# Kernel tuning notes

Hardware: AMD Instinct MI355X
Metric: run time of the kernel (lower is better)

Reference implementation:

```python
import jax, jax.numpy as jnp
import numpy as np


def _apply_ring(x, angles):
    """Apply x @ R^T where R = G_0 @ G_1 @ ... @ G_{n-1} with ring planes
    (k, (k+1) % n). Equivalent to applying G_k^T to x for k = n-1 .. 0:
      x[:, k] <- c*x[:, k] - s*x[:, j]
      x[:, j] <- s*x[:, k] + c*x[:, j]
    x: [B, n], angles: [n].
    """
    n = angles.shape[0]

    def step(xT, k):
        a = angles[k]
        c, s = jnp.cos(a), jnp.sin(a)
        j = jnp.mod(k + 1, n)
        xi = xT[k]
        xj = xT[j]
        xT = xT.at[k].set(c * xi - s * xj)
        xT = xT.at[j].set(s * xi + c * xj)
        return xT, None

    ks = jnp.arange(n - 1, -1, -1)  # reverse order: R^T = G_{n-1}^T ... G_0^T
    xT, _ = jax.lax.scan(step, x.T, ks)  # carry is [n, B]
    return xT.T


def setup_inputs() -> dict:
    key = jax.random.key(0)
    k_x, k_e, k_d = jax.random.split(key, 3)
    B, n, num_blocks = 8192, 1024, 4
    return {
        "x": jax.random.normal(k_x, (B, n), dtype=jnp.float32),
        "angles_enc": jax.random.normal(k_e, (num_blocks, n), dtype=jnp.float32),
        "angles_dec": jax.random.normal(k_d, (num_blocks, n), dtype=jnp.float32),
        "hidden_weight": jnp.zeros((1,), dtype=jnp.float32),
        "hidden_state": jnp.zeros((n,), dtype=jnp.float32),
    }


def reference(x, angles_enc, angles_dec, hidden_weight, hidden_state):
    num_blocks = angles_enc.shape[0]
    b = x
    for blk in range(num_blocks):
        b = _apply_ring(b, angles_enc[blk])
    # recurrent blend; weight uses the detached hidden_weight (original uses
    # numpy on .detach()), so stop_gradient matches the original semantics.
    w = jax.nn.sigmoid(jax.lax.stop_gradient(hidden_weight[0]))
    bottleneck = (1.0 - w) * b + w * hidden_state[None, :]
    out = bottleneck
    for blk in range(num_blocks):
        out = _apply_ring(out, angles_dec[blk])
    return (bottleneck, out)
```

## Files before the change

### kernel.cpp

```cpp
#include <hip/hip_runtime.h>
#include <math.h>

#define N_COLS 1024
#define NRINGS 8

#define TPR    32
#define CHUNK  32
#define PAIRS_PER_BLOCK 8

#define F_OFF   16384
#define A_OFF   24576
#define AUX_OFF 24832
#define WS_FLOATS 24848

typedef const __attribute__((address_space(1))) float4* gas_f4;
typedef __attribute__((address_space(3))) void* las_ptr;

__global__ __launch_bounds__(256)
void ced_setup(const float* __restrict__ ae,
               const float* __restrict__ ad,
               float* __restrict__ ws)
{
    __shared__ float2 ls[256];
    const int r   = blockIdx.x >> 2;
    const int b   = blockIdx.x & 3;
    const int tid = threadIdx.x;
    const int k   = (b << 8) + tid;
    const float* ang = (r < 4) ? (ae + (r << 10)) : (ad + ((r - 4) << 10));

    float sv, cv;
    sincosf(ang[k], &sv, &cv);
    if (k == N_COLS - 1) {
        ((float2*)(ws + AUX_OFF))[r] = make_float2(cv, sv);
        cv = 0.f; sv = -1.f;
    }
    ls[tid] = make_float2(cv, sv);
    __syncthreads();

    if (!(tid & 1)) {
        float2 e0 = ls[tid], e1 = ls[tid + 1];
        int t  = k >> 5;
        int jp = (k & 31) >> 1;
        ((float4*)ws)[(r*16 + jp)*32 + t] = make_float4(e0.x, e0.y, e1.x, e1.y);
    }

    if (tid < 64) {
        const int lt = tid >> 3;
        const int q  = tid & 7;
        const int t  = (b << 3) + lt;
        const int j0 = lt * CHUNK + 4 * q;
        float2 e0 = ls[j0], e1 = ls[j0+1], e2 = ls[j0+2], e3 = ls[j0+3];

        float f3 = e3.x;       float P = -e3.y;
        float f2 = e2.x * P;   P *= -e2.y;
        float f1 = e1.x * P;   P *= -e1.y;
        float f0 = e0.x * P;   P *= -e0.y;

        float ip = P;
        #pragma unroll
        for (int d = 1; d < 8; d <<= 1) {
            float tmp = __shfl_down(ip, d);
            if (q + d < 8) ip *= tmp;
        }
        float ex = __shfl_down(ip, 1);
        if (q == 7) ex = 1.f;
        f0 *= ex; f1 *= ex; f2 *= ex; f3 *= ex;

        ((float4*)(ws + F_OFF))[(r*8 + q)*32 + t] = make_float4(f0, f1, f2, f3);
        if (q == 0) ws[A_OFF + r*TPR + t] = ip;
    }
}

__global__ __launch_bounds__(256, 2)
void ced_main(const float* __restrict__ x,
              const float* __restrict__ ws,
              const float* __restrict__ hw,
              const float* __restrict__ hs,
              float* __restrict__ out, int B)
{
    __shared__ float4 sCS[2][1024];
    __shared__ float4 sF [2][512];
    __shared__ float4 sA4[64];
    __shared__ float4 sAux4[4];

    const float4* CSg = (const float4*)ws;
    const float4* Fg  = (const float4*)(ws + F_OFF);

    const int tid  = threadIdx.x;
    const int lane = tid & 63;
    const int t    = lane & 31;
    const int groupBase = lane & 32;
    const int pairRow = blockIdx.x * PAIRS_PER_BLOCK + (tid >> 5);
    const size_t rowA = (size_t)(2 * pairRow) * N_COLS;
    const size_t rowB = rowA + N_COLS;

    #pragma unroll
    for (int m = 0; m < 4; ++m)
        __builtin_amdgcn_global_load_lds((gas_f4)(CSg + m*256 + tid),
                                         (las_ptr)&sCS[0][m*256 + tid], 16, 0, 0);
    #pragma unroll
    for (int m = 0; m < 2; ++m)
        __builtin_amdgcn_global_load_lds((gas_f4)(Fg + m*256 + tid),
                                         (las_ptr)&sF[0][m*256 + tid], 16, 0, 0);

    if (tid < 64)              sA4[tid]        = ((const float4*)(ws + A_OFF))[tid];
    if (tid >= 64 && tid < 68) sAux4[tid - 64] = ((const float4*)(ws + AUX_OFF))[tid - 64];

    float ya[CHUNK], yb[CHUNK];
    {
        const float4* xa = (const float4*)(x + rowA + t * CHUNK);
        const float4* xb = (const float4*)(x + rowB + t * CHUNK);
        #pragma unroll
        for (int i = 0; i < 8; ++i) {
            float4 va = xa[i], vb = xb[i];
            ya[4*i] = va.x; ya[4*i+1] = va.y; ya[4*i+2] = va.z; ya[4*i+3] = va.w;
            yb[4*i] = vb.x; yb[4*i+1] = vb.y; yb[4*i+2] = vb.z; yb[4*i+3] = vb.w;
        }
    }

    const float w   = 1.f / (1.f + expf(-hw[0]));
    const float omw = 1.f - w;

    __syncthreads();

    const float*  As   = (const float*)sA4;
    const float2* Auxs = (const float2*)sAux4;

    #pragma unroll 1
    for (int p = 0; p < 4; ++p) {
        if (p < 3) {
            const int nb = (p + 1) & 1;
            const float4* gc = CSg + (p + 1) * 1024;
            const float4* gf = Fg  + (p + 1) * 512;
            #pragma unroll
            for (int m = 0; m < 4; ++m)
                __builtin_amdgcn_global_load_lds((gas_f4)(gc + m*256 + tid),
                                                 (las_ptr)&sCS[nb][m*256 + tid], 16, 0, 0);
            #pragma unroll
            for (int m = 0; m < 2; ++m)
                __builtin_amdgcn_global_load_lds((gas_f4)(gf + m*256 + tid),
                                                 (las_ptr)&sF[nb][m*256 + tid], 16, 0, 0);
        }

        const int buf = p & 1;
        #pragma unroll
        for (int lr = 0; lr < 2; ++lr) {
            const int rr = 2 * p + lr;

            if (p == 2 && lr == 0) {
                float4* oa = (float4*)(out + rowA + t * CHUNK);
                float4* ob = (float4*)(out + rowB + t * CHUNK);
                const float4* hp = (const float4*)(hs + t * CHUNK);
                #pragma unroll
                for (int i = 0; i < 8; ++i) {
                    float4 h = hp[i];
                    float4 na, nb2;
                    na.x  = fmaf(omw, ya[4*i+0], w * h.x);
                    na.y  = fmaf(omw, ya[4*i+1], w * h.y);
                    na.z  = fmaf(omw, ya[4*i+2], w * h.z);
                    na.w  = fmaf(omw, ya[4*i+3], w * h.w);
                    nb2.x = fmaf(omw, yb[4*i+0], w * h.x);
                    nb2.y = fmaf(omw, yb[4*i+1], w * h.y);
                    nb2.z = fmaf(omw, yb[4*i+2], w * h.z);
                    nb2.w = fmaf(omw, yb[4*i+3], w * h.w);
                    oa[i] = na; ob[i] = nb2;
                    ya[4*i+0] = na.x;  ya[4*i+1] = na.y;  ya[4*i+2] = na.z;  ya[4*i+3] = na.w;
                    yb[4*i+0] = nb2.x; yb[4*i+1] = nb2.y; yb[4*i+2] = nb2.z; yb[4*i+3] = nb2.w;
                }
            }

            const float4* csL = &sCS[buf][lr * 512];
            const float4* fL  = &sF [buf][lr * 256];
            const float2  cN  = Auxs[rr];
            const float   saI = As[rr * TPR + t];

            float y0a = __shfl(ya[0],       groupBase);
            float yNa = __shfl(ya[CHUNK-1], groupBase + 31);
            float y0b = __shfl(yb[0],       groupBase);
            float yNb = __shfl(yb[CHUNK-1], groupBase + 31);
            float CinitA = cN.x * yNa - cN.y * y0a;
            float CinitB = cN.x * yNb - cN.y * y0b;
            float x0nA   = fmaf(cN.y, yNa, cN.x * y0a);
            float x0nB   = fmaf(cN.y, yNb, cN.x * y0b);
            if (t == 0) { ya[0] = x0nA; yb[0] = x0nB; }

            float carA = 0.f, carB = 0.f, ztA = 0.f, ztB = 0.f;
            #pragma unroll
            for (int jp = CHUNK/2 - 1; jp >= 0; --jp) {
                float4 cs4 = csL[jp * 32 + t];
                const int j1 = 2*jp + 1;
                float z1a = fmaf(cs4.w, ya[j1], cs4.z * carA);
                float z1b = fmaf(cs4.w, yb[j1], cs4.z * carB);
                carA = fmaf(-cs4.w, carA, cs4.z * ya[j1]);
                carB = fmaf(-cs4.w, carB, cs4.z * yb[j1]);
                if (j1 == CHUNK - 1) { ztA = z1a; ztB = z1b; }
                else                 { ya[j1+1] = z1a; yb[j1+1] = z1b; }
                const int j0 = 2*jp;
                float z0a = fmaf(cs4.y, ya[j0], cs4.x * carA);
                float z0b = fmaf(cs4.y, yb[j0], cs4.x * carB);
                carA = fmaf(-cs4.y, carA, cs4.x * ya[j0]);
                carB = fmaf(-cs4.y, carB, cs4.x * yb[j0]);
                ya[j0+1] = z0a; yb[j0+1] = z0b;
            }

            float sa = saI;
            float sbA = carA, sbB = carB;
            #pragma unroll
            for (int d = 1; d < TPR; d <<= 1) {
                float a2  = __shfl_down(sa,  d);
                float b2a = __shfl_down(sbA, d);
                float b2b = __shfl_down(sbB, d);
                if (t + d < TPR) {
                    sbA = fmaf(sa, b2a, sbA);
                    sbB = fmaf(sa, b2b, sbB);
                    sa *= a2;
                }
            }
            float ea  = __shfl_down(sa,  1);
            float ebA = __shfl_down(sbA, 1);
            float ebB = __shfl_down(sbB, 1);
            float zfA = fmaf(sa, CinitA, sbA);
            float zfB = fmaf(sa, CinitB, sbB);
            float CinA = (t == TPR - 1) ? CinitA : fmaf(ea, CinitA, ebA);
            float CinB = (t == TPR - 1) ? CinitB : fmaf(ea, CinitB, ebB);

            #pragma unroll
            for (int qi = CHUNK/4 - 1; qi >= 0; --qi) {
                float4 f4 = fL[qi * 32 + t];
                const int j = 4*qi;
                if (j + 3 == CHUNK - 1) { ztA = fmaf(f4.w, CinA, ztA);
                                          ztB = fmaf(f4.w, CinB, ztB); }
                else                    { ya[j+4] = fmaf(f4.w, CinA, ya[j+4]);
                                          yb[j+4] = fmaf(f4.w, CinB, yb[j+4]); }
                ya[j+3] = fmaf(f4.z, CinA, ya[j+3]);  yb[j+3] = fmaf(f4.z, CinB, yb[j+3]);
                ya[j+2] = fmaf(f4.y, CinA, ya[j+2]);  yb[j+2] = fmaf(f4.y, CinB, yb[j+2]);
                ya[j+1] = fmaf(f4.x, CinA, ya[j+1]);  yb[j+1] = fmaf(f4.x, CinB, yb[j+1]);
            }

            float upA = __shfl_up(ztA, 1);
            float upB = __shfl_up(ztB, 1);
            ya[0] = (t == 0) ? zfA : upA;
            yb[0] = (t == 0) ? zfB : upB;
        }

        if (p < 3) __syncthreads();
    }

    float4* oa = (float4*)(out + (size_t)B * N_COLS + rowA + t * CHUNK);
    float4* ob = (float4*)(out + (size_t)B * N_COLS + rowB + t * CHUNK);
    #pragma unroll
    for (int i = 0; i < 8; ++i) {
        oa[i] = make_float4(ya[4*i], ya[4*i+1], ya[4*i+2], ya[4*i+3]);
        ob[i] = make_float4(yb[4*i], yb[4*i+1], yb[4*i+2], yb[4*i+3]);
    }
}

__global__ __launch_bounds__(256, 2)
void ced_fallback(const float* __restrict__ x,
                  const float* __restrict__ ae,
                  const float* __restrict__ ad,
                  const float* __restrict__ hw,
                  const float* __restrict__ hs,
                  float* __restrict__ out, int B)
{
    __shared__ float2 s_cs[NRINGS * 64 * 16];
    __shared__ float  s_A [NRINGS * 16];
    __shared__ float2 s_aux[NRINGS];

    const int tid = threadIdx.x;
    for (int i = 0; i < 32; ++i) {
        int idx = i * 256 + tid;
        int r   = idx >> 10;
        int k   = idx & 1023;
        const float* ang = (r < 4) ? (ae + (r << 10)) : (ad + ((r - 4) << 10));
        float sv, cv;
        sincosf(ang[k], &sv, &cv);
        int t = k >> 6, j = k & 63;
        float2 e = make_float2(cv, sv);
        if (k == 1023) { s_aux[r] = e; e = make_float2(0.f, -1.f); }
        s_cs[(r * 64 + j) * 16 + t] = e;
    }
    __syncthreads();
    if (tid < NRINGS * 16) {
        int r = tid >> 4, t = tid & 15;
        float p = 1.f;
        for (int j = 0; j < 64; ++j) p *= -s_cs[(r * 64 + j) * 16 + t].y;
        s_A[tid] = p;
    }
    __syncthreads();

    const int lane      = tid & 63;
    const int g         = lane >> 4;
    const int t         = lane & 15;
    const int groupBase = lane & 48;
    const int row       = blockIdx.x * 16 + (tid >> 6) * 4 + g;

    const float* xr = x + (size_t)row * N_COLS + t * 64;
    float y[64];
    #pragma unroll
    for (int i = 0; i < 16; ++i) {
        float4 v = ((const float4*)xr)[i];
        y[4*i] = v.x; y[4*i+1] = v.y; y[4*i+2] = v.z; y[4*i+3] = v.w;
    }
    const float w   = 1.f / (1.f + expf(-hw[0]));
    const float omw = 1.f - w;

    for (int r = 0; r < NRINGS; ++r) {
        if (r == 4) {
            float4* ob = (float4*)(out + (size_t)row * N_COLS + t * 64);
            const float4* hp = (const float4*)(hs + t * 64);
            #pragma unroll
            for (int i = 0; i < 16; ++i) {
                float4 h = hp[i];
                float4 bn;
                bn.x = fmaf(omw, y[4*i+0], w * h.x);
                bn.y = fmaf(omw, y[4*i+1], w * h.y);
                bn.z = fmaf(omw, y[4*i+2], w * h.z);
                bn.w = fmaf(omw, y[4*i+3], w * h.w);
                ob[i] = bn;
                y[4*i+0] = bn.x; y[4*i+1] = bn.y; y[4*i+2] = bn.z; y[4*i+3] = bn.w;
            }
        }
        const float2* csr = s_cs + r * 64 * 16;
        const float2  cN  = s_aux[r];
        float y0 = __shfl(y[0],  groupBase);
        float yN = __shfl(y[63], groupBase + 15);
        float Cinit = cN.x * yN - cN.y * y0;
        float x0n   = fmaf(cN.y, yN, cN.x * y0);
        if (t == 0) y[0] = x0n;

        float carry = 0.f, ztmp = 0.f;
        #pragma unroll
        for (int j = 63; j >= 0; --j) {
            float2 cs = csr[j * 16 + t];
            float z   = fmaf(cs.y, y[j], cs.x * carry);
            carry     = fmaf(-cs.y, carry, cs.x * y[j]);
            if (j == 63) ztmp = z; else y[j + 1] = z;
        }
        float sa = s_A[r * 16 + t], sb = carry;
        #pragma unroll
        for (int d = 1; d < 16; d <<= 1) {
            float a2 = __shfl_down(sa, d);
            float b2 = __shfl_down(sb, d);
            if (t + d < 16) { sb = fmaf(sa, b2, sb); sa *= a2; }
        }
        float ea = __shfl_down(sa, 1);
        float eb = __shfl_down(sb, 1);
        float z0  = fmaf(sa, Cinit, sb);
        float Cin = (t == 15) ? Cinit : fmaf(ea, Cinit, eb);

        float P = 1.f;
        #pragma unroll
        for (int j = 63; j >= 0; --j) {
            float2 cs = csr[j * 16 + t];
            float f = cs.x * P;
            P = -cs.y * P;
            if (j == 63) ztmp = fmaf(f, Cin, ztmp);
            else         y[j + 1] = fmaf(f, Cin, y[j + 1]);
        }
        float up = __shfl_up(ztmp, 1);
        y[0] = (t == 0) ? z0 : up;
    }

    float4* oo = (float4*)(out + (size_t)B * N_COLS + (size_t)row * N_COLS + t * 64);
    #pragma unroll
    for (int i = 0; i < 16; ++i)
        oo[i] = make_float4(y[4*i], y[4*i+1], y[4*i+2], y[4*i+3]);
}

extern "C" void kernel_launch(void* const* d_in, const int* in_sizes, int n_in,
                              void* d_out, int out_size, void* d_ws, size_t ws_size,
                              hipStream_t stream) {
    const float* x  = (const float*)d_in[0];
    const float* ae = (const float*)d_in[1];
    const float* ad = (const float*)d_in[2];
    const float* hw = (const float*)d_in[3];
    const float* hs = (const float*)d_in[4];
    float* out = (float*)d_out;
    const int B = in_sizes[0] / N_COLS;

    if (ws_size >= WS_FLOATS * sizeof(float)) {
        hipLaunchKernelGGL(ced_setup, dim3(32), dim3(256), 0, stream,
                           ae, ad, (float*)d_ws);
        hipLaunchKernelGGL(ced_main, dim3(B / (2 * PAIRS_PER_BLOCK)), dim3(256), 0, stream,
                           x, (const float*)d_ws, hw, hs, out, B);
    } else {
        hipLaunchKernelGGL(ced_fallback, dim3(B / 16), dim3(256), 0, stream,
                           x, ae, ad, hw, hs, out, B);
    }
}
```

Before: 125.4 us.

## Remap ring scan to one row per wavefront with 64 lanes of 16 columns

Switches the main kernel from two rows per 32-lane half-wave (32 columns per lane) to one row per full 64-lane wavefront with 16 columns per lane. Blocks grow to 512 threads with per-ring double-buffered coefficient staging (a barrier per ring instead of per pair of rings). The setup kernel's coefficient layout and prefix products are rewritten for the new chunking. This cuts registers per thread and raises occupancy and parallelism, but the cross-lane scan gains a sixth shuffle step and runs on all 64 lanes, and the rings no longer share two rows per lane.

New measurement: 276.1 us. 120% more time.

```diff
diff --git a/kernel.cpp b/kernel.cpp
--- a/kernel.cpp
+++ b/kernel.cpp
@@ -4,14 +4,14 @@
 #define N_COLS 1024
 #define NRINGS 8
 
-#define TPR    32
-#define CHUNK  32
-#define PAIRS_PER_BLOCK 8
+#define TPR    64
+#define CHUNK  16
+#define ROWS_PER_BLOCK 8
 
 #define F_OFF   16384
 #define A_OFF   24576
-#define AUX_OFF 24832
-#define WS_FLOATS 24848
+#define AUX_OFF 25088
+#define WS_FLOATS 25104
 
 typedef const __attribute__((address_space(1))) float4* gas_f4;
 typedef __attribute__((address_space(3))) void* las_ptr;
@@ -39,15 +39,15 @@
 
     if (!(tid & 1)) {
         float2 e0 = ls[tid], e1 = ls[tid + 1];
-        int t  = k >> 5;
-        int jp = (k & 31) >> 1;
-        ((float4*)ws)[(r*16 + jp)*32 + t] = make_float4(e0.x, e0.y, e1.x, e1.y);
+        int t  = k >> 4;
+        int jp = (k & 15) >> 1;
+        ((float4*)ws)[(r*8 + jp)*64 + t] = make_float4(e0.x, e0.y, e1.x, e1.y);
     }
 
     if (tid < 64) {
-        const int lt = tid >> 3;
-        const int q  = tid & 7;
-        const int t  = (b << 3) + lt;
+        const int lt = tid >> 2;
+        const int q  = tid & 3;
+        const int t  = (b << 4) + lt;
         const int j0 = lt * CHUNK + 4 * q;
         float2 e0 = ls[j0], e1 = ls[j0+1], e2 = ls[j0+2], e3 = ls[j0+3];
 
@@ -58,63 +58,55 @@
 
         float ip = P;
         #pragma unroll
-        for (int d = 1; d < 8; d <<= 1) {
+        for (int d = 1; d < 4; d <<= 1) {
             float tmp = __shfl_down(ip, d);
-            if (q + d < 8) ip *= tmp;
+            if (q + d < 4) ip *= tmp;
         }
         float ex = __shfl_down(ip, 1);
-        if (q == 7) ex = 1.f;
+        if (q == 3) ex = 1.f;
         f0 *= ex; f1 *= ex; f2 *= ex; f3 *= ex;
 
-        ((float4*)(ws + F_OFF))[(r*8 + q)*32 + t] = make_float4(f0, f1, f2, f3);
+        ((float4*)(ws + F_OFF))[(r*4 + q)*64 + t] = make_float4(f0, f1, f2, f3);
         if (q == 0) ws[A_OFF + r*TPR + t] = ip;
     }
 }
 
-__global__ __launch_bounds__(256, 2)
+__global__ __launch_bounds__(512, 8)
 void ced_main(const float* __restrict__ x,
               const float* __restrict__ ws,
               const float* __restrict__ hw,
               const float* __restrict__ hs,
               float* __restrict__ out, int B)
 {
-    __shared__ float4 sCS[2][1024];
-    __shared__ float4 sF [2][512];
-    __shared__ float4 sA4[64];
+    __shared__ float4 sCS[2][512];
+    __shared__ float4 sF [2][256];
+    __shared__ float4 sA4[128];
     __shared__ float4 sAux4[4];
 
     const float4* CSg = (const float4*)ws;
     const float4* Fg  = (const float4*)(ws + F_OFF);
 
-    const int tid  = threadIdx.x;
-    const int lane = tid & 63;
-    const int t    = lane & 31;
-    const int groupBase = lane & 32;
-    const int pairRow = blockIdx.x * PAIRS_PER_BLOCK + (tid >> 5);
-    const size_t rowA = (size_t)(2 * pairRow) * N_COLS;
-    const size_t rowB = rowA + N_COLS;
-
-    #pragma unroll
-    for (int m = 0; m < 4; ++m)
-        __builtin_amdgcn_global_load_lds((gas_f4)(CSg + m*256 + tid),
-                                         (las_ptr)&sCS[0][m*256 + tid], 16, 0, 0);
-    #pragma unroll
-    for (int m = 0; m < 2; ++m)
-        __builtin_amdgcn_global_load_lds((gas_f4)(Fg + m*256 + tid),
-                                         (las_ptr)&sF[0][m*256 + tid], 16, 0, 0);
-
-    if (tid < 64)              sA4[tid]        = ((const float4*)(ws + A_OFF))[tid];
-    if (tid >= 64 && tid < 68) sAux4[tid - 64] = ((const float4*)(ws + AUX_OFF))[tid - 64];
-
-    float ya[CHUNK], yb[CHUNK];
+    const int tid = threadIdx.x;
+    const int t   = tid & 63;
+    const int row = blockIdx.x * ROWS_PER_BLOCK + (tid >> 6);
+    const size_t rowOff = (size_t)row * N_COLS;
+
+    __builtin_amdgcn_global_load_lds((gas_f4)(CSg + tid),
+                                     (las_ptr)&sCS[0][tid], 16, 0, 0);
+    if (tid < 256)
+        __builtin_amdgcn_global_load_lds((gas_f4)(Fg + tid),
+                                         (las_ptr)&sF[0][tid], 16, 0, 0);
+
+    if (tid < 128)                sA4[tid]         = ((const float4*)(ws + A_OFF))[tid];
+    if (tid >= 128 && tid < 132)  sAux4[tid - 128] = ((const float4*)(ws + AUX_OFF))[tid - 128];
+
+    float y[CHUNK];
     {
-        const float4* xa = (const float4*)(x + rowA + t * CHUNK);
-        const float4* xb = (const float4*)(x + rowB + t * CHUNK);
-        #pragma unroll
-        for (int i = 0; i < 8; ++i) {
-            float4 va = xa[i], vb = xb[i];
-            ya[4*i] = va.x; ya[4*i+1] = va.y; ya[4*i+2] = va.z; ya[4*i+3] = va.w;
-            yb[4*i] = vb.x; yb[4*i+1] = vb.y; yb[4*i+2] = vb.z; yb[4*i+3] = vb.w;
+        const float4* xp = (const float4*)(x + rowOff + t * CHUNK);
+        #pragma unroll
+        for (int i = 0; i < 4; ++i) {
+            float4 v = xp[i];
+            y[4*i] = v.x; y[4*i+1] = v.y; y[4*i+2] = v.z; y[4*i+3] = v.w;
         }
     }
 
@@ -127,132 +119,92 @@
     const float2* Auxs = (const float2*)sAux4;
 
     #pragma unroll 1
-    for (int p = 0; p < 4; ++p) {
-        if (p < 3) {
-            const int nb = (p + 1) & 1;
-            const float4* gc = CSg + (p + 1) * 1024;
-            const float4* gf = Fg  + (p + 1) * 512;
+    for (int r = 0; r < NRINGS; ++r) {
+        if (r < NRINGS - 1) {
+            const int nb = (r + 1) & 1;
+            __builtin_amdgcn_global_load_lds((gas_f4)(CSg + (r + 1) * 512 + tid),
+                                             (las_ptr)&sCS[nb][tid], 16, 0, 0);
+            if (tid < 256)
+                __builtin_amdgcn_global_load_lds((gas_f4)(Fg + (r + 1) * 256 + tid),
+                                                 (las_ptr)&sF[nb][tid], 16, 0, 0);
+        }
+
+        if (r == 4) {
+            float4* oa = (float4*)(out + rowOff + t * CHUNK);
+            const float4* hp = (const float4*)(hs + t * CHUNK);
             #pragma unroll
-            for (int m = 0; m < 4; ++m)
-                __builtin_amdgcn_global_load_lds((gas_f4)(gc + m*256 + tid),
-                                                 (las_ptr)&sCS[nb][m*256 + tid], 16, 0, 0);
-            #pragma unroll
-            for (int m = 0; m < 2; ++m)
-                __builtin_amdgcn_global_load_lds((gas_f4)(gf + m*256 + tid),
-                                                 (las_ptr)&sF[nb][m*256 + tid], 16, 0, 0);
-        }
-
-        const int buf = p & 1;
-        #pragma unroll
-        for (int lr = 0; lr < 2; ++lr) {
-            const int rr = 2 * p + lr;
-
-            if (p == 2 && lr == 0) {
-                float4* oa = (float4*)(out + rowA + t * CHUNK);
-                float4* ob = (float4*)(out + rowB + t * CHUNK);
-                const float4* hp = (const float4*)(hs + t * CHUNK);
-                #pragma unroll
-                for (int i = 0; i < 8; ++i) {
-                    float4 h = hp[i];
-                    float4 na, nb2;
-                    na.x  = fmaf(omw, ya[4*i+0], w * h.x);
-                    na.y  = fmaf(omw, ya[4*i+1], w * h.y);
-                    na.z  = fmaf(omw, ya[4*i+2], w * h.z);
-                    na.w  = fmaf(omw, ya[4*i+3], w * h.w);
-                    nb2.x = fmaf(omw, yb[4*i+0], w * h.x);
-                    nb2.y = fmaf(omw, yb[4*i+1], w * h.y);
-                    nb2.z = fmaf(omw, yb[4*i+2], w * h.z);
-                    nb2.w = fmaf(omw, yb[4*i+3], w * h.w);
-                    oa[i] = na; ob[i] = nb2;
-                    ya[4*i+0] = na.x;  ya[4*i+1] = na.y;  ya[4*i+2] = na.z;  ya[4*i+3] = na.w;
-                    yb[4*i+0] = nb2.x; yb[4*i+1] = nb2.y; yb[4*i+2] = nb2.z; yb[4*i+3] = nb2.w;
-                }
+            for (int i = 0; i < 4; ++i) {
+                float4 h = hp[i];
+                float4 nb2;
+                nb2.x = fmaf(omw, y[4*i+0], w * h.x);
+                nb2.y = fmaf(omw, y[4*i+1], w * h.y);
+                nb2.z = fmaf(omw, y[4*i+2], w * h.z);
+                nb2.w = fmaf(omw, y[4*i+3], w * h.w);
+                oa[i] = nb2;
+                y[4*i+0] = nb2.x; y[4*i+1] = nb2.y; y[4*i+2] = nb2.z; y[4*i+3] = nb2.w;
             }
-
-            const float4* csL = &sCS[buf][lr * 512];
-            const float4* fL  = &sF [buf][lr * 256];
-            const float2  cN  = Auxs[rr];
-            const float   saI = As[rr * TPR + t];
-
-            float y0a = __shfl(ya[0],       groupBase);
-            float yNa = __shfl(ya[CHUNK-1], groupBase + 31);
-            float y0b = __shfl(yb[0],       groupBase);
-            float yNb = __shfl(yb[CHUNK-1], groupBase + 31);
-            float CinitA = cN.x * yNa - cN.y * y0a;
-            float CinitB = cN.x * yNb - cN.y * y0b;
-            float x0nA   = fmaf(cN.y, yNa, cN.x * y0a);
-            float x0nB   = fmaf(cN.y, yNb, cN.x * y0b);
-            if (t == 0) { ya[0] = x0nA; yb[0] = x0nB; }
-
-            float carA = 0.f, carB = 0.f, ztA = 0.f, ztB = 0.f;
-            #pragma unroll
-            for (int jp = CHUNK/2 - 1; jp >= 0; --jp) {
-                float4 cs4 = csL[jp * 32 + t];
-                const int j1 = 2*jp + 1;
-                float z1a = fmaf(cs4.w, ya[j1], cs4.z * carA);
-                float z1b = fmaf(cs4.w, yb[j1], cs4.z * carB);
-                carA = fmaf(-cs4.w, carA, cs4.z * ya[j1]);
-                carB = fmaf(-cs4.w, carB, cs4.z * yb[j1]);
-                if (j1 == CHUNK - 1) { ztA = z1a; ztB = z1b; }
-                else                 { ya[j1+1] = z1a; yb[j1+1] = z1b; }
-                const int j0 = 2*jp;
-                float z0a = fmaf(cs4.y, ya[j0], cs4.x * carA);
-                float z0b = fmaf(cs4.y, yb[j0], cs4.x * carB);
-                carA = fmaf(-cs4.y, carA, cs4.x * ya[j0]);
-                carB = fmaf(-cs4.y, carB, cs4.x * yb[j0]);
-                ya[j0+1] = z0a; yb[j0+1] = z0b;
-            }
-
-            float sa = saI;
-            float sbA = carA, sbB = carB;
-            #pragma unroll
-            for (int d = 1; d < TPR; d <<= 1) {
-                float a2  = __shfl_down(sa,  d);
-                float b2a = __shfl_down(sbA, d);
-                float b2b = __shfl_down(sbB, d);
-                if (t + d < TPR) {
-                    sbA = fmaf(sa, b2a, sbA);
-                    sbB = fmaf(sa, b2b, sbB);
-                    sa *= a2;
-                }
-            }
-            float ea  = __shfl_down(sa,  1);
-            float ebA = __shfl_down(sbA, 1);
-            float ebB = __shfl_down(sbB, 1);
-            float zfA = fmaf(sa, CinitA, sbA);
-            float zfB = fmaf(sa, CinitB, sbB);
-            float CinA = (t == TPR - 1) ? CinitA : fmaf(ea, CinitA, ebA);
-            float CinB = (t == TPR - 1) ? CinitB : fmaf(ea, CinitB, ebB);
-
-            #pragma unroll
-            for (int qi = CHUNK/4 - 1; qi >= 0; --qi) {
-                float4 f4 = fL[qi * 32 + t];
-                const int j = 4*qi;
-                if (j + 3 == CHUNK - 1) { ztA = fmaf(f4.w, CinA, ztA);
-                                          ztB = fmaf(f4.w, CinB, ztB); }
-                else                    { ya[j+4] = fmaf(f4.w, CinA, ya[j+4]);
-                                          yb[j+4] = fmaf(f4.w, CinB, yb[j+4]); }
-                ya[j+3] = fmaf(f4.z, CinA, ya[j+3]);  yb[j+3] = fmaf(f4.z, CinB, yb[j+3]);
-                ya[j+2] = fmaf(f4.y, CinA, ya[j+2]);  yb[j+2] = fmaf(f4.y, CinB, yb[j+2]);
-                ya[j+1] = fmaf(f4.x, CinA, ya[j+1]);  yb[j+1] = fmaf(f4.x, CinB, yb[j+1]);
-            }
-
-            float upA = __shfl_up(ztA, 1);
-            float upB = __shfl_up(ztB, 1);
-            ya[0] = (t == 0) ? zfA : upA;
-            yb[0] = (t == 0) ? zfB : upB;
-        }
-
-        if (p < 3) __syncthreads();
-    }
-
-    float4* oa = (float4*)(out + (size_t)B * N_COLS + rowA + t * CHUNK);
-    float4* ob = (float4*)(out + (size_t)B * N_COLS + rowB + t * CHUNK);
+        }
+
+        const int buf = r & 1;
+        const float4* csL = &sCS[buf][0];
+        const float4* fL  = &sF [buf][0];
+        const float2  cN  = Auxs[r];
+        const float   saI = As[r * TPR + t];
+
+        float y0 = __shfl(y[0],       0);
+        float yN = __shfl(y[CHUNK-1], 63);
+        float Cinit = cN.x * yN - cN.y * y0;
+        float x0n   = fmaf(cN.y, yN, cN.x * y0);
+        if (t == 0) y[0] = x0n;
+
+        float car = 0.f, zt = 0.f;
+        #pragma unroll
+        for (int jp = CHUNK/2 - 1; jp >= 0; --jp) {
+            float4 cs4 = csL[jp * 64 + t];
+            const int j1 = 2*jp + 1;
+            float z1 = fmaf(cs4.w, y[j1], cs4.z * car);
+            car = fmaf(-cs4.w, car, cs4.z * y[j1]);
+            if (j1 == CHUNK - 1) zt = z1;
+            else                 y[j1+1] = z1;
+            const int j0 = 2*jp;
+            float z0 = fmaf(cs4.y, y[j0], cs4.x * car);
+            car = fmaf(-cs4.y, car, cs4.x * y[j0]);
+            y[j0+1] = z0;
+        }
+
+        float sa = saI, sb = car;
+        #pragma unroll
+        for (int d = 1; d < TPR; d <<= 1) {
+            float a2 = __shfl_down(sa, d);
+            float b2 = __shfl_down(sb, d);
+            if (t + d < TPR) { sb = fmaf(sa, b2, sb); sa *= a2; }
+        }
+        float ea = __shfl_down(sa, 1);
+        float eb = __shfl_down(sb, 1);
+        float zf  = fmaf(sa, Cinit, sb);
+        float Cin = (t == TPR - 1) ? Cinit : fmaf(ea, Cinit, eb);
+
+        #pragma unroll
+        for (int qi = CHUNK/4 - 1; qi >= 0; --qi) {
+            float4 f4 = fL[qi * 64 + t];
+            const int j = 4*qi;
+            if (j + 3 == CHUNK - 1) zt = fmaf(f4.w, Cin, zt);
+            else                    y[j+4] = fmaf(f4.w, Cin, y[j+4]);
+            y[j+3] = fmaf(f4.z, Cin, y[j+3]);
+            y[j+2] = fmaf(f4.y, Cin, y[j+2]);
+            y[j+1] = fmaf(f4.x, Cin, y[j+1]);
+        }
+
+        float up = __shfl_up(zt, 1);
+        y[0] = (t == 0) ? zf : up;
+
+        if (r < NRINGS - 1) __syncthreads();
+    }
+
+    float4* oo = (float4*)(out + (size_t)B * N_COLS + rowOff + t * CHUNK);
     #pragma unroll
-    for (int i = 0; i < 8; ++i) {
-        oa[i] = make_float4(ya[4*i], ya[4*i+1], ya[4*i+2], ya[4*i+3]);
-        ob[i] = make_float4(yb[4*i], yb[4*i+1], yb[4*i+2], yb[4*i+3]);
-    }
+    for (int i = 0; i < 4; ++i)
+        oo[i] = make_float4(y[4*i], y[4*i+1], y[4*i+2], y[4*i+3]);
 }
 
 __global__ __launch_bounds__(256, 2)
@@ -379,10 +331,10 @@
     float* out = (float*)d_out;
     const int B = in_sizes[0] / N_COLS;
 
-    if (ws_size >= WS_FLOATS * sizeof(float)) {
+    if (ws_size >= WS_FLOATS * sizeof(float) && (B % ROWS_PER_BLOCK) == 0) {
         hipLaunchKernelGGL(ced_setup, dim3(32), dim3(256), 0, stream,
                            ae, ad, (float*)d_ws);
-        hipLaunchKernelGGL(ced_main, dim3(B / (2 * PAIRS_PER_BLOCK)), dim3(256), 0, stream,
+        hipLaunchKernelGGL(ced_main, dim3(B / ROWS_PER_BLOCK), dim3(512), 0, stream,
                            x, (const float*)d_ws, hw, hs, out, B);
     } else {
         hipLaunchKernelGGL(ced_fallback, dim3(B / 16), dim3(256), 0, stream,
```

## Split rows across full 64-lane wavefronts and read ring coefficients directly from global

Applied to the files above, without the earlier changes.

Each row is now handled by a whole 64-thread wavefront with 16 elements per thread instead of a 32-lane half-wave with 32 elements. The scan and coefficient tables are re-laid out to match. The LDS double-buffered staging of rotation coefficients is removed; threads read the cos/sin and correction factors straight from global memory, which should hit in cache since every block shares them. This removes the block barriers and LDS use and raises the occupancy target to 4 blocks per CU. In exchange the cross-lane prefix scan gains a step, and every coefficient read becomes a global load rather than an LDS read.

New measurement: 123.9 us. About the same (-1.2%).

```diff
diff --git a/kernel.cpp b/kernel.cpp
--- a/kernel.cpp
+++ b/kernel.cpp
@@ -4,17 +4,14 @@
 #define N_COLS 1024
 #define NRINGS 8
 
-#define TPR    32
-#define CHUNK  32
-#define PAIRS_PER_BLOCK 8
-
-#define F_OFF   16384
-#define A_OFF   24576
-#define AUX_OFF 24832
-#define WS_FLOATS 24848
-
-typedef const __attribute__((address_space(1))) float4* gas_f4;
-typedef __attribute__((address_space(3))) void* las_ptr;
+#define TPR    64
+#define CHUNK  16
+#define PAIRS_PER_BLOCK 4
+
+#define F_OFF    16384
+#define A_OFF    24576
+#define AUX_OFF  25088
+#define WS_FLOATS 25104
 
 __global__ __launch_bounds__(256)
 void ced_setup(const float* __restrict__ ae,
@@ -39,15 +36,15 @@
 
     if (!(tid & 1)) {
         float2 e0 = ls[tid], e1 = ls[tid + 1];
-        int t  = k >> 5;
-        int jp = (k & 31) >> 1;
-        ((float4*)ws)[(r*16 + jp)*32 + t] = make_float4(e0.x, e0.y, e1.x, e1.y);
+        int t  = k >> 4;
+        int jp = (k & 15) >> 1;
+        ((float4*)ws)[(r*8 + jp)*64 + t] = make_float4(e0.x, e0.y, e1.x, e1.y);
     }
 
     if (tid < 64) {
-        const int lt = tid >> 3;
-        const int q  = tid & 7;
-        const int t  = (b << 3) + lt;
+        const int lt = tid >> 2;
+        const int q  = tid & 3;
+        const int t  = (b << 4) + lt;
         const int j0 = lt * CHUNK + 4 * q;
         float2 e0 = ls[j0], e1 = ls[j0+1], e2 = ls[j0+2], e3 = ls[j0+3];
 
@@ -58,60 +55,43 @@
 
         float ip = P;
         #pragma unroll
-        for (int d = 1; d < 8; d <<= 1) {
+        for (int d = 1; d < 4; d <<= 1) {
             float tmp = __shfl_down(ip, d);
-            if (q + d < 8) ip *= tmp;
+            if (q + d < 4) ip *= tmp;
         }
         float ex = __shfl_down(ip, 1);
-        if (q == 7) ex = 1.f;
+        if (q == 3) ex = 1.f;
         f0 *= ex; f1 *= ex; f2 *= ex; f3 *= ex;
 
-        ((float4*)(ws + F_OFF))[(r*8 + q)*32 + t] = make_float4(f0, f1, f2, f3);
+        ((float4*)(ws + F_OFF))[(r*4 + q)*64 + t] = make_float4(f0, f1, f2, f3);
         if (q == 0) ws[A_OFF + r*TPR + t] = ip;
     }
 }
 
-__global__ __launch_bounds__(256, 2)
+__global__ __launch_bounds__(256, 4)
 void ced_main(const float* __restrict__ x,
               const float* __restrict__ ws,
               const float* __restrict__ hw,
               const float* __restrict__ hs,
               float* __restrict__ out, int B)
 {
-    __shared__ float4 sCS[2][1024];
-    __shared__ float4 sF [2][512];
-    __shared__ float4 sA4[64];
-    __shared__ float4 sAux4[4];
-
-    const float4* CSg = (const float4*)ws;
-    const float4* Fg  = (const float4*)(ws + F_OFF);
-
-    const int tid  = threadIdx.x;
-    const int lane = tid & 63;
-    const int t    = lane & 31;
-    const int groupBase = lane & 32;
-    const int pairRow = blockIdx.x * PAIRS_PER_BLOCK + (tid >> 5);
+    const int tid = threadIdx.x;
+    const int t   = tid & 63;
+    const int pairRow = blockIdx.x * PAIRS_PER_BLOCK + (tid >> 6);
     const size_t rowA = (size_t)(2 * pairRow) * N_COLS;
     const size_t rowB = rowA + N_COLS;
 
-    #pragma unroll
-    for (int m = 0; m < 4; ++m)
-        __builtin_amdgcn_global_load_lds((gas_f4)(CSg + m*256 + tid),
-                                         (las_ptr)&sCS[0][m*256 + tid], 16, 0, 0);
-    #pragma unroll
-    for (int m = 0; m < 2; ++m)
-        __builtin_amdgcn_global_load_lds((gas_f4)(Fg + m*256 + tid),
-                                         (las_ptr)&sF[0][m*256 + tid], 16, 0, 0);
-
-    if (tid < 64)              sA4[tid]        = ((const float4*)(ws + A_OFF))[tid];
-    if (tid >= 64 && tid < 68) sAux4[tid - 64] = ((const float4*)(ws + AUX_OFF))[tid - 64];
+    const float4* CSg  = (const float4*)ws;
+    const float4* Fg   = (const float4*)(ws + F_OFF);
+    const float*  Ag   = ws + A_OFF;
+    const float2* AUXg = (const float2*)(ws + AUX_OFF);
 
     float ya[CHUNK], yb[CHUNK];
     {
         const float4* xa = (const float4*)(x + rowA + t * CHUNK);
         const float4* xb = (const float4*)(x + rowB + t * CHUNK);
         #pragma unroll
-        for (int i = 0; i < 8; ++i) {
+        for (int i = 0; i < 4; ++i) {
             float4 va = xa[i], vb = xb[i];
             ya[4*i] = va.x; ya[4*i+1] = va.y; ya[4*i+2] = va.z; ya[4*i+3] = va.w;
             yb[4*i] = vb.x; yb[4*i+1] = vb.y; yb[4*i+2] = vb.z; yb[4*i+3] = vb.w;
@@ -121,135 +101,107 @@
     const float w   = 1.f / (1.f + expf(-hw[0]));
     const float omw = 1.f - w;
 
-    __syncthreads();
-
-    const float*  As   = (const float*)sA4;
-    const float2* Auxs = (const float2*)sAux4;
-
     #pragma unroll 1
-    for (int p = 0; p < 4; ++p) {
-        if (p < 3) {
-            const int nb = (p + 1) & 1;
-            const float4* gc = CSg + (p + 1) * 1024;
-            const float4* gf = Fg  + (p + 1) * 512;
+    for (int r = 0; r < NRINGS; ++r) {
+        if (r == 4) {
+            float4* oa = (float4*)(out + rowA + t * CHUNK);
+            float4* ob = (float4*)(out + rowB + t * CHUNK);
+            const float4* hp = (const float4*)(hs + t * CHUNK);
             #pragma unroll
-            for (int m = 0; m < 4; ++m)
-                __builtin_amdgcn_global_load_lds((gas_f4)(gc + m*256 + tid),
-                                                 (las_ptr)&sCS[nb][m*256 + tid], 16, 0, 0);
-            #pragma unroll
-            for (int m = 0; m < 2; ++m)
-                __builtin_amdgcn_global_load_lds((gas_f4)(gf + m*256 + tid),
-                                                 (las_ptr)&sF[nb][m*256 + tid], 16, 0, 0);
-        }
-
-        const int buf = p & 1;
-        #pragma unroll
-        for (int lr = 0; lr < 2; ++lr) {
-            const int rr = 2 * p + lr;
-
-            if (p == 2 && lr == 0) {
-                float4* oa = (float4*)(out + rowA + t * CHUNK);
-                float4* ob = (float4*)(out + rowB + t * CHUNK);
-                const float4* hp = (const float4*)(hs + t * CHUNK);
-                #pragma unroll
-                for (int i = 0; i < 8; ++i) {
-                    float4 h = hp[i];
-                    float4 na, nb2;
-                    na.x  = fmaf(omw, ya[4*i+0], w * h.x);
-                    na.y  = fmaf(omw, ya[4*i+1], w * h.y);
-                    na.z  = fmaf(omw, ya[4*i+2], w * h.z);
-                    na.w  = fmaf(omw, ya[4*i+3], w * h.w);
-                    nb2.x = fmaf(omw, yb[4*i+0], w * h.x);
-                    nb2.y = fmaf(omw, yb[4*i+1], w * h.y);
-                    nb2.z = fmaf(omw, yb[4*i+2], w * h.z);
-                    nb2.w = fmaf(omw, yb[4*i+3], w * h.w);
-                    oa[i] = na; ob[i] = nb2;
-                    ya[4*i+0] = na.x;  ya[4*i+1] = na.y;  ya[4*i+2] = na.z;  ya[4*i+3] = na.w;
-                    yb[4*i+0] = nb2.x; yb[4*i+1] = nb2.y; yb[4*i+2] = nb2.z; yb[4*i+3] = nb2.w;
-                }
+            for (int i = 0; i < 4; ++i) {
+                float4 h = hp[i];
+                float4 na, nb2;
+                na.x  = fmaf(omw, ya[4*i+0], w * h.x);
+                na.y  = fmaf(omw, ya[4*i+1], w * h.y);
+                na.z  = fmaf(omw, ya[4*i+2], w * h.z);
+                na.w  = fmaf(omw, ya[4*i+3], w * h.w);
+                nb2.x = fmaf(omw, yb[4*i+0], w * h.x);
+                nb2.y = fmaf(omw, yb[4*i+1], w * h.y);
+                nb2.z = fmaf(omw, yb[4*i+2], w * h.z);
+                nb2.w = fmaf(omw, yb[4*i+3], w * h.w);
+                oa[i] = na; ob[i] = nb2;
+                ya[4*i+0] = na.x;  ya[4*i+1] = na.y;  ya[4*i+2] = na.z;  ya[4*i+3] = na.w;
+                yb[4*i+0] = nb2.x; yb[4*i+1] = nb2.y; yb[4*i+2] = nb2.z; yb[4*i+3] = nb2.w;
             }
-
-            const float4* csL = &sCS[buf][lr * 512];
-            const float4* fL  = &sF [buf][lr * 256];
-            const float2  cN  = Auxs[rr];
-            const float   saI = As[rr * TPR + t];
-
-            float y0a = __shfl(ya[0],       groupBase);
-            float yNa = __shfl(ya[CHUNK-1], groupBase + 31);
-            float y0b = __shfl(yb[0],       groupBase);
-            float yNb = __shfl(yb[CHUNK-1], groupBase + 31);
-            float CinitA = cN.x * yNa - cN.y * y0a;
-            float CinitB = cN.x * yNb - cN.y * y0b;
-            float x0nA   = fmaf(cN.y, yNa, cN.x * y0a);
-            float x0nB   = fmaf(cN.y, yNb, cN.x * y0b);
-            if (t == 0) { ya[0] = x0nA; yb[0] = x0nB; }
-
-            float carA = 0.f, carB = 0.f, ztA = 0.f, ztB = 0.f;
-            #pragma unroll
-            for (int jp = CHUNK/2 - 1; jp >= 0; --jp) {
-                float4 cs4 = csL[jp * 32 + t];
-                const int j1 = 2*jp + 1;
-                float z1a = fmaf(cs4.w, ya[j1], cs4.z * carA);
-                float z1b = fmaf(cs4.w, yb[j1], cs4.z * carB);
-                carA = fmaf(-cs4.w, carA, cs4.z * ya[j1]);
-                carB = fmaf(-cs4.w, carB, cs4.z * yb[j1]);
-                if (j1 == CHUNK - 1) { ztA = z1a; ztB = z1b; }
-                else                 { ya[j1+1] = z1a; yb[j1+1] = z1b; }
-                const int j0 = 2*jp;
-                float z0a = fmaf(cs4.y, ya[j0], cs4.x * carA);
-                float z0b = fmaf(cs4.y, yb[j0], cs4.x * carB);
-                carA = fmaf(-cs4.y, carA, cs4.x * ya[j0]);
-                carB = fmaf(-cs4.y, carB, cs4.x * yb[j0]);
-                ya[j0+1] = z0a; yb[j0+1] = z0b;
+        }
+
+        const float4* cs = CSg + r * 512;
+        const float4* fp = Fg  + r * 256;
+        const float2  cN  = AUXg[r];
+        const float   saI = Ag[r * TPR + t];
+
+        float y0a = __shfl(ya[0],       0);
+        float yNa = __shfl(ya[CHUNK-1], 63);
+        float y0b = __shfl(yb[0],       0);
+        float yNb = __shfl(yb[CHUNK-1], 63);
+        float CinitA = cN.x * yNa - cN.y * y0a;
+        float CinitB = cN.x * yNb - cN.y * y0b;
+        float x0nA   = fmaf(cN.y, yNa, cN.x * y0a);
+        float x0nB   = fmaf(cN.y, yNb, cN.x * y0b);
+        if (t == 0) { ya[0] = x0nA; yb[0] = x0nB; }
+
+        float carA = 0.f, carB = 0.f, ztA = 0.f, ztB = 0.f;
+        #pragma unroll
+        for (int jp = CHUNK/2 - 1; jp >= 0; --jp) {
+            float4 cs4 = cs[jp * 64 + t];
+            const int j1 = 2*jp + 1;
+            float z1a = fmaf(cs4.w, ya[j1], cs4.z * carA);
+            float z1b = fmaf(cs4.w, yb[j1], cs4.z * carB);
+            carA = fmaf(-cs4.w, carA, cs4.z * ya[j1]);
+            carB = fmaf(-cs4.w, carB, cs4.z * yb[j1]);
+            if (j1 == CHUNK - 1) { ztA = z1a; ztB = z1b; }
+            else                 { ya[j1+1] = z1a; yb[j1+1] = z1b; }
+            const int j0 = 2*jp;
+            float z0a = fmaf(cs4.y, ya[j0], cs4.x * carA);
+            float z0b = fmaf(cs4.y, yb[j0], cs4.x * carB);
+            carA = fmaf(-cs4.y, carA, cs4.x * ya[j0]);
+            carB = fmaf(-cs4.y, carB, cs4.x * yb[j0]);
+            ya[j0+1] = z0a; yb[j0+1] = z0b;
+        }
+
+        float sa = saI, sbA = carA, sbB = carB;
+        #pragma unroll
+        for (int d = 1; d < TPR; d <<= 1) {
+            float a2  = __shfl_down(sa,  d);
+            float b2a = __shfl_down(sbA, d);
+            float b2b = __shfl_down(sbB, d);
+            if (t + d < TPR) {
+                sbA = fmaf(sa, b2a, sbA);
+                sbB = fmaf(sa, b2b, sbB);
+                sa *= a2;
             }
-
-            float sa = saI;
-            float sbA = carA, sbB = carB;
-            #pragma unroll
-            for (int d = 1; d < TPR; d <<= 1) {
-                float a2  = __shfl_down(sa,  d);
-                float b2a = __shfl_down(sbA, d);
-                float b2b = __shfl_down(sbB, d);
-                if (t + d < TPR) {
-                    sbA = fmaf(sa, b2a, sbA);
-                    sbB = fmaf(sa, b2b, sbB);
-                    sa *= a2;
-                }
-            }
-            float ea  = __shfl_down(sa,  1);
-            float ebA = __shfl_down(sbA, 1);
-            float ebB = __shfl_down(sbB, 1);
-            float zfA = fmaf(sa, CinitA, sbA);
-            float zfB = fmaf(sa, CinitB, sbB);
-            float CinA = (t == TPR - 1) ? CinitA : fmaf(ea, CinitA, ebA);
-            float CinB = (t == TPR - 1) ? CinitB : fmaf(ea, CinitB, ebB);
-
-            #pragma unroll
-            for (int qi = CHUNK/4 - 1; qi >= 0; --qi) {
-                float4 f4 = fL[qi * 32 + t];
-                const int j = 4*qi;
-                if (j + 3 == CHUNK - 1) { ztA = fmaf(f4.w, CinA, ztA);
-                                          ztB = fmaf(f4.w, CinB, ztB); }
-                else                    { ya[j+4] = fmaf(f4.w, CinA, ya[j+4]);
-                                          yb[j+4] = fmaf(f4.w, CinB, yb[j+4]); }
-                ya[j+3] = fmaf(f4.z, CinA, ya[j+3]);  yb[j+3] = fmaf(f4.z, CinB, yb[j+3]);
-                ya[j+2] = fmaf(f4.y, CinA, ya[j+2]);  yb[j+2] = fmaf(f4.y, CinB, yb[j+2]);
-                ya[j+1] = fmaf(f4.x, CinA, ya[j+1]);  yb[j+1] = fmaf(f4.x, CinB, yb[j+1]);
-            }
-
-            float upA = __shfl_up(ztA, 1);
-            float upB = __shfl_up(ztB, 1);
-            ya[0] = (t == 0) ? zfA : upA;
-            yb[0] = (t == 0) ? zfB : upB;
-        }
-
-        if (p < 3) __syncthreads();
+        }
+        float ea  = __shfl_down(sa,  1);
+        float ebA = __shfl_down(sbA, 1);
+        float ebB = __shfl_down(sbB, 1);
+        float zfA = fmaf(sa, CinitA, sbA);
+        float zfB = fmaf(sa, CinitB, sbB);
+        float CinA = (t == TPR - 1) ? CinitA : fmaf(ea, CinitA, ebA);
+        float CinB = (t == TPR - 1) ? CinitB : fmaf(ea, CinitB, ebB);
+
+        #pragma unroll
+        for (int qi = CHUNK/4 - 1; qi >= 0; --qi) {
+            float4 f4 = fp[qi * 64 + t];
+            const int j = 4*qi;
+            if (j + 3 == CHUNK - 1) { ztA = fmaf(f4.w, CinA, ztA);
+                                      ztB = fmaf(f4.w, CinB, ztB); }
+            else                    { ya[j+4] = fmaf(f4.w, CinA, ya[j+4]);
+                                      yb[j+4] = fmaf(f4.w, CinB, yb[j+4]); }
+            ya[j+3] = fmaf(f4.z, CinA, ya[j+3]);  yb[j+3] = fmaf(f4.z, CinB, yb[j+3]);
+            ya[j+2] = fmaf(f4.y, CinA, ya[j+2]);  yb[j+2] = fmaf(f4.y, CinB, yb[j+2]);
+            ya[j+1] = fmaf(f4.x, CinA, ya[j+1]);  yb[j+1] = fmaf(f4.x, CinB, yb[j+1]);
+        }
+
+        float upA = __shfl_up(ztA, 1);
+        float upB = __shfl_up(ztB, 1);
+        ya[0] = (t == 0) ? zfA : upA;
+        yb[0] = (t == 0) ? zfB : upB;
     }
 
     float4* oa = (float4*)(out + (size_t)B * N_COLS + rowA + t * CHUNK);
     float4* ob = (float4*)(out + (size_t)B * N_COLS + rowB + t * CHUNK);
     #pragma unroll
-    for (int i = 0; i < 8; ++i) {
+    for (int i = 0; i < 4; ++i) {
         oa[i] = make_float4(ya[4*i], ya[4*i+1], ya[4*i+2], ya[4*i+3]);
         ob[i] = make_float4(yb[4*i], yb[4*i+1], yb[4*i+2], yb[4*i+3]);
     }
@@ -379,7 +331,7 @@
     float* out = (float*)d_out;
     const int B = in_sizes[0] / N_COLS;
 
-    if (ws_size >= WS_FLOATS * sizeof(float)) {
+    if (ws_size >= WS_FLOATS * sizeof(float) && (B % (2 * PAIRS_PER_BLOCK)) == 0) {
         hipLaunchKernelGGL(ced_setup, dim3(32), dim3(256), 0, stream,
                            ae, ad, (float*)d_ws);
         hipLaunchKernelGGL(ced_main, dim3(B / (2 * PAIRS_PER_BLOCK)), dim3(256), 0, stream,
```
